# Optimization experiments

Measured on AMD Instinct MI355X. Metric: run time of the kernel, lower is better.

Reference implementation:

```python
import jax, jax.numpy as jnp
import numpy as np

D_MODEL = 2048
SSM_RANK = 8            # ultra_config.ar_ssm_max_rank = 8
FFN_RANK = D_MODEL // 64  # = 32, UltraLowRankFFN default rank
EPS = 1e-5


def setup_inputs() -> dict:
    key = jax.random.key(0)
    ks = jax.random.split(key, 10)
    d, r, rf = D_MODEL, SSM_RANK, FFN_RANK
    sc = 0.01  # xavier-ish small gain init mirroring gain=0.01
    return {
        "x": jax.random.normal(ks[0], (4, 4096, d), dtype=jnp.float32),
        # shared LayerNorm (used for both pre-norms)
        "ln_gamma": jnp.ones((d,), jnp.float32),
        "ln_beta": jnp.zeros((d,), jnp.float32),
        # AR-SSM (adaptive-rank semiseparable): input proj, per-rank decay, output proj, skip D
        "W_in": jax.random.normal(ks[1], (d, r), jnp.float32) * (1.0 / np.sqrt(d)),
        "b_in": jnp.zeros((r,), jnp.float32),
        "decay_logit": jax.random.normal(ks[2], (r,), jnp.float32),
        "W_out": jax.random.normal(ks[3], (r, d), jnp.float32) * (1.0 / np.sqrt(r)),
        "b_out": jnp.zeros((d,), jnp.float32),
        "D_skip": jax.random.normal(ks[4], (d,), jnp.float32) * 0.1,
        # Ultra low-rank FFN
        "W_down": jax.random.normal(ks[5], (d, rf), jnp.float32) * sc,
        "b_down": jnp.zeros((rf,), jnp.float32),
        "W_up": jax.random.normal(ks[6], (rf, d), jnp.float32) * sc,
        "b_up": jnp.zeros((d,), jnp.float32),
    }


def _layernorm(x, gamma, beta):
    mu = jnp.mean(x, axis=-1, keepdims=True)
    var = jnp.var(x, axis=-1, keepdims=True)
    return (x - mu) * jax.lax.rsqrt(var + EPS) * gamma + beta


def _ssm_scan(u, decay):
    # h_t = decay * h_{t-1} + u_t ; u: [B,S,r], decay: [r]
    a = jnp.broadcast_to(decay, u.shape)

    def combine(e1, e2):
        a1, b1 = e1
        a2, b2 = e2
        return a1 * a2, a2 * b1 + b2

    _, h = jax.lax.associative_scan(combine, (a, u), axis=1)
    return h  # [B,S,r]


def reference(x, ln_gamma, ln_beta, W_in, b_in, decay_logit, W_out, b_out,
              D_skip, W_down, b_down, W_up, b_up):
    # --- AR-SSM sub-block (pre-norm) ---
    xn = _layernorm(x, ln_gamma, ln_beta)
    u = jnp.einsum("bsd,dr->bsr", xn, W_in) + b_in          # low-rank input proj
    decay = jax.nn.sigmoid(decay_logit)                       # per-rank decay in (0,1)
    h = _ssm_scan(u, decay)                                   # semiseparable scan
    x_ar = jnp.einsum("bsr,rd->bsd", h, W_out) + b_out + xn * D_skip
    x = x + x_ar
    # --- Ultra low-rank FFN sub-block (same shared norm) ---
    xn2 = _layernorm(x, ln_gamma, ln_beta)
    hf = jax.nn.relu(jnp.einsum("bsd,dr->bsr", xn2, W_down) + b_down)
    x_ffn = jnp.einsum("bsr,rd->bsd", hf, W_up) + b_up
    return x + x_ffn
```

## Files before the change

### kernel.cpp

```cpp
#include <hip/hip_runtime.h>
#include <cstdint>
#include <cstddef>

#define D_MODEL 2048
#define EPSF 1e-5f

#define WS_UT    0
#define WS_MU1   131072
#define WS_RSIG1 147456
#define WS_WDT   163840
#define WS_WINF  229376
#define WS_C     245760
#define WS_D     245792
#define WS_CIN   245824
#define WS_DIN   245832

__device__ __forceinline__ float4 ld4(const float* __restrict__ p) {
    return *(const float4*)p;
}
__device__ __forceinline__ void st4(float* __restrict__ p, float4 v) {
    *(float4*)p = v;
}
__device__ __forceinline__ int bitrev6(int l) {
    return ((l & 1) << 5) | ((l & 2) << 3) | ((l & 4) << 1) |
           ((l & 8) >> 1) | ((l & 16) >> 3) | ((l & 32) >> 5);
}
__device__ __forceinline__ int bitrev4(int l) {
    return ((l & 1) << 3) | ((l & 2) << 1) | ((l & 4) >> 1) | ((l & 8) >> 3);
}

__global__ __launch_bounds__(64) void k0_prep(
    const float* __restrict__ Win, const float* __restrict__ b_in,
    const float* __restrict__ Wd, const float* __restrict__ gamma,
    const float* __restrict__ beta, const float* __restrict__ bd,
    float* __restrict__ ws)
{
    const int t = threadIdx.x;
    const int blk = blockIdx.x;
    if (blk < 8) {
        __shared__ float tile[64 * 33];
        const int gblk = blk;
        for (int cc = 0; cc < 4; ++cc) {
            const int ibase = gblk * 256 + cc * 64;
#pragma unroll
            for (int m = 0; m < 32; ++m) {
                const int e = m * 64 + t;
                const int il = e >> 5, j = e & 31;
                tile[il * 33 + j] = Wd[(size_t)ibase * 32 + e];
            }
            __syncthreads();
#pragma unroll
            for (int j = 0; j < 32; ++j) {
                const int i = ibase + t;
                ws[WS_WDT + (size_t)j * 2048 + i] = gamma[i] * tile[t * 33 + j];
            }
            __syncthreads();
        }
    } else if (blk == 8) {
        const int j = t & 31, h = t >> 5;
        float cacc = 0.f, dacc = 0.f;
        for (int k = 0; k < 1024; ++k) {
            const int i = h * 1024 + k;
            const float w = Wd[(size_t)i * 32 + j];
            cacc = fmaf(gamma[i], w, cacc);
            dacc = fmaf(beta[i], w, dacc);
        }
        cacc += __shfl_xor(cacc, 32, 64);
        dacc += __shfl_xor(dacc, 32, 64);
        if (t < 32) {
            ws[WS_C + j] = cacc;
            ws[WS_D + j] = dacc + bd[j];
        }
    } else {
        float cj[8], dj[8];
#pragma unroll
        for (int j = 0; j < 8; ++j) { cj[j] = 0.f; dj[j] = 0.f; }
        for (int k = 0; k < 32; ++k) {
            const int i = k * 64 + t;
            const float g = gamma[i], b = beta[i];
            float4 w0 = ld4(Win + (size_t)i * 8);
            float4 w1 = ld4(Win + (size_t)i * 8 + 4);
            st4(ws + WS_WINF + (size_t)i * 8,
                make_float4(g * w0.x, g * w0.y, g * w0.z, g * w0.w));
            st4(ws + WS_WINF + (size_t)i * 8 + 4,
                make_float4(g * w1.x, g * w1.y, g * w1.z, g * w1.w));
            cj[0] = fmaf(g, w0.x, cj[0]); cj[1] = fmaf(g, w0.y, cj[1]);
            cj[2] = fmaf(g, w0.z, cj[2]); cj[3] = fmaf(g, w0.w, cj[3]);
            cj[4] = fmaf(g, w1.x, cj[4]); cj[5] = fmaf(g, w1.y, cj[5]);
            cj[6] = fmaf(g, w1.z, cj[6]); cj[7] = fmaf(g, w1.w, cj[7]);
            dj[0] = fmaf(b, w0.x, dj[0]); dj[1] = fmaf(b, w0.y, dj[1]);
            dj[2] = fmaf(b, w0.z, dj[2]); dj[3] = fmaf(b, w0.w, dj[3]);
            dj[4] = fmaf(b, w1.x, dj[4]); dj[5] = fmaf(b, w1.y, dj[5]);
            dj[6] = fmaf(b, w1.z, dj[6]); dj[7] = fmaf(b, w1.w, dj[7]);
        }
#pragma unroll
        for (int off = 1; off < 64; off <<= 1) {
#pragma unroll
            for (int j = 0; j < 8; ++j) {
                cj[j] += __shfl_xor(cj[j], off, 64);
                dj[j] += __shfl_xor(dj[j], off, 64);
            }
        }
        if (t == 0) {
#pragma unroll
            for (int j = 0; j < 8; ++j) {
                ws[WS_CIN + j] = cj[j];
                ws[WS_DIN + j] = dj[j] + b_in[j];
            }
        }
    }
}

__global__ __launch_bounds__(256, 4) void k1_ln_u(
    const float* __restrict__ x, float* __restrict__ ws)
{
    __shared__ float red[8][4][12];
    const int t = threadIdx.x;
    const int wv = t >> 6, lane = t & 63;
    const int row0 = blockIdx.x * 8;
    const int i0 = t * 8;

    float winf[64];
#pragma unroll
    for (int q = 0; q < 16; ++q) {
        float4 v = ld4(ws + WS_WINF + (size_t)i0 * 8 + q * 4);
        winf[q*4+0] = v.x; winf[q*4+1] = v.y; winf[q*4+2] = v.z; winf[q*4+3] = v.w;
    }
    float4 xa = ld4(x + (size_t)row0 * D_MODEL + i0);
    float4 xb = ld4(x + (size_t)row0 * D_MODEL + i0 + 4);
#pragma unroll 1
    for (int rr = 0; rr < 8; ++rr) {
        float xc[8];
        xc[0]=xa.x; xc[1]=xa.y; xc[2]=xa.z; xc[3]=xa.w;
        xc[4]=xb.x; xc[5]=xb.y; xc[6]=xb.z; xc[7]=xb.w;
        if (rr < 7) {
            const float* xr = x + (size_t)(row0 + rr + 1) * D_MODEL + i0;
            xa = ld4(xr);
            xb = ld4(xr + 4);
        }
        float vals[16];
#pragma unroll
        for (int v = 0; v < 16; ++v) vals[v] = 0.f;
#pragma unroll
        for (int i = 0; i < 8; ++i) {
            const float xi = xc[i];
            vals[0] += xi;
            vals[1] = fmaf(xi, xi, vals[1]);
#pragma unroll
            for (int j = 0; j < 8; ++j)
                vals[2+j] = fmaf(xi, winf[i*8 + j], vals[2+j]);
        }
        int count = 16;
#pragma unroll
        for (int step = 1; step <= 32; step <<= 1) {
            if (count > 1) {
                const int half = count >> 1;
                const bool up = (lane & step) != 0;
#pragma unroll
                for (int k = 0; k < 8; ++k) {
                    if (k < half) {
                        float send = vals[up ? k : k + half];
                        float keep = vals[up ? k + half : k];
                        vals[k] = keep + __shfl_xor(send, step, 64);
                    }
                }
                count = half;
            } else {
                vals[0] += __shfl_xor(vals[0], step, 64);
            }
        }
        if (lane < 16) {
            const int v = bitrev4(lane);
            if (v < 10) red[rr][wv][v] = vals[0];
        }
    }
    __syncthreads();
    if (t < 64) {
        const int row = t >> 3, j = t & 7;
        float s_ = 0.f, q_ = 0.f, uraw = 0.f;
#pragma unroll
        for (int w = 0; w < 4; ++w) {
            s_   += red[row][w][0];
            q_   += red[row][w][1];
            uraw += red[row][w][2 + j];
        }
        const float mu = s_ * (1.f / D_MODEL);
        const float var = q_ * (1.f / D_MODEL) - mu * mu;
        const float rs = rsqrtf(var + EPSF);
        const float u = fmaf(rs, fmaf(-mu, ws[WS_CIN + j], uraw), ws[WS_DIN + j]);
        const int grow = row0 + row;
        const int bb = grow >> 12, s0 = grow & 4095;
        ws[WS_UT + ((size_t)bb * 8 + j) * 4096 + s0] = u;
        if (j == 0) {
            ws[WS_MU1 + grow] = mu;
            ws[WS_RSIG1 + grow] = rs;
        }
    }
}

__global__ __launch_bounds__(64) void k2_scan(
    const float* __restrict__ logit, float* __restrict__ ws)
{
    const int t = threadIdx.x;
    const int blk = blockIdx.x;
    const int b = blk >> 3, r = blk & 7;
    const float a = 1.f / (1.f + expf(-logit[r]));
    float* u = ws + WS_UT + ((size_t)b * 8 + r) * 4096 + t * 64;
    float v[64];
#pragma unroll
    for (int q = 0; q < 16; ++q) {
        float4 w = ld4(u + q * 4);
        v[q*4]=w.x; v[q*4+1]=w.y; v[q*4+2]=w.z; v[q*4+3]=w.w;
    }
    float c = 0.f;
#pragma unroll
    for (int k = 0; k < 64; ++k) { c = fmaf(a, c, v[k]); v[k] = c; }
    float A = a;
#pragma unroll
    for (int i = 0; i < 6; ++i) A *= A;
    float Bv = c, Aa = A;
#pragma unroll
    for (int off = 1; off < 64; off <<= 1) {
        float Ap = __shfl_up(Aa, off, 64);
        float Bp = __shfl_up(Bv, off, 64);
        if (t >= off) { Bv = fmaf(Aa, Bp, Bv); Aa *= Ap; }
    }
    float P = __shfl_up(Bv, 1, 64);
    if (t == 0) P = 0.f;
    float f = a * P;
#pragma unroll
    for (int k = 0; k < 64; ++k) { v[k] += f; f *= a; }
#pragma unroll
    for (int q = 0; q < 16; ++q)
        st4(u + q * 4, make_float4(v[q*4], v[q*4+1], v[q*4+2], v[q*4+3]));
}

__global__ __launch_bounds__(256, 2) void k3_fused(
    const float* __restrict__ x, const float* __restrict__ gamma,
    const float* __restrict__ beta, const float* __restrict__ Wout,
    const float* __restrict__ b_out, const float* __restrict__ Dsk,
    const float* __restrict__ Wu, const float* __restrict__ bu,
    float* __restrict__ out, float* __restrict__ ws)
{
    __shared__ float Y[8 * 2048];
    __shared__ float sh_h[8][8];
    __shared__ float smu1[8], srs1[8];
    __shared__ float smu2[8], srs2[8];
    __shared__ float red2[16][4];
    __shared__ float shf[8 * 32];
    const int t = threadIdx.x;
    const int blk = blockIdx.x;
    const int row0 = blk * 8;
    const int wv = t >> 6, lane = t & 63;

    if (t < 64) {
        const int r_ = t >> 3, j_ = t & 7;
        const int grow = row0 + r_;
        const int bb = grow >> 12, s = grow & 4095;
        sh_h[r_][j_] = ws[WS_UT + ((size_t)bb * 8 + j_) * 4096 + s];
        if (j_ == 0) {
            smu1[r_] = ws[WS_MU1 + grow];
            srs1[r_] = ws[WS_RSIG1 + grow];
        }
    }
    __syncthreads();

    float hreg[64];
#pragma unroll
    for (int r = 0; r < 8; ++r) {
        float4 h0 = ld4(&sh_h[r][0]);
        float4 h1 = ld4(&sh_h[r][4]);
        hreg[r*8+0]=h0.x; hreg[r*8+1]=h0.y; hreg[r*8+2]=h0.z; hreg[r*8+3]=h0.w;
        hreg[r*8+4]=h1.x; hreg[r*8+5]=h1.y; hreg[r*8+6]=h1.z; hreg[r*8+7]=h1.w;
    }

    float sum[8], ssq[8];
#pragma unroll
    for (int r = 0; r < 8; ++r) { sum[r] = 0.f; ssq[r] = 0.f; }

#pragma unroll 1
    for (int pass = 0; pass < 2; ++pass) {
        const int c = pass * 1024 + t * 4;
        const float4 g = ld4(gamma + c), bt = ld4(beta + c);
        const float4 bo = ld4(b_out + c), dk = ld4(Dsk + c);
        float4 wo[8];
#pragma unroll
        for (int j = 0; j < 8; ++j) wo[j] = ld4(Wout + (size_t)j * D_MODEL + c);
#pragma unroll
        for (int r = 0; r < 8; ++r) {
            const float4 xv = ld4(x + (size_t)(row0 + r) * D_MODEL + c);
            const float mu1 = smu1[r], rs1 = srs1[r];
            float4 acc = bo;
#pragma unroll
            for (int j = 0; j < 8; ++j) {
                const float hj = hreg[r*8 + j];
                acc.x = fmaf(hj, wo[j].x, acc.x);
                acc.y = fmaf(hj, wo[j].y, acc.y);
                acc.z = fmaf(hj, wo[j].z, acc.z);
                acc.w = fmaf(hj, wo[j].w, acc.w);
            }
            float4 xn;
            xn.x = fmaf((xv.x - mu1) * rs1, g.x, bt.x);
            xn.y = fmaf((xv.y - mu1) * rs1, g.y, bt.y);
            xn.z = fmaf((xv.z - mu1) * rs1, g.z, bt.z);
            xn.w = fmaf((xv.w - mu1) * rs1, g.w, bt.w);
            acc.x = fmaf(xn.x, dk.x, acc.x);
            acc.y = fmaf(xn.y, dk.y, acc.y);
            acc.z = fmaf(xn.z, dk.z, acc.z);
            acc.w = fmaf(xn.w, dk.w, acc.w);
            float4 x2;
            x2.x = xv.x + acc.x; x2.y = xv.y + acc.y;
            x2.z = xv.z + acc.z; x2.w = xv.w + acc.w;
            st4(&Y[r * 2048 + c], x2);
            sum[r] += x2.x + x2.y + x2.z + x2.w;
            ssq[r] = fmaf(x2.x, x2.x, ssq[r]); ssq[r] = fmaf(x2.y, x2.y, ssq[r]);
            ssq[r] = fmaf(x2.z, x2.z, ssq[r]); ssq[r] = fmaf(x2.w, x2.w, ssq[r]);
        }
    }
    {
        float vals[16];
#pragma unroll
        for (int r = 0; r < 8; ++r) { vals[r] = sum[r]; vals[8+r] = ssq[r]; }
        int count = 16;
#pragma unroll
        for (int step = 1; step <= 32; step <<= 1) {
            if (count > 1) {
                const int half = count >> 1;
                const bool up = (lane & step) != 0;
#pragma unroll
                for (int k = 0; k < 8; ++k) {
                    if (k < half) {
                        float send = vals[up ? k : k + half];
                        float keep = vals[up ? k + half : k];
                        vals[k] = keep + __shfl_xor(send, step, 64);
                    }
                }
                count = half;
            } else {
                vals[0] += __shfl_xor(vals[0], step, 64);
            }
        }
        if (lane < 16) red2[bitrev4(lane)][wv] = vals[0];
    }
    __syncthreads();
    if (t < 8) {
        float s_ = red2[t][0] + red2[t][1] + red2[t][2] + red2[t][3];
        float q_ = red2[8+t][0] + red2[8+t][1] + red2[8+t][2] + red2[8+t][3];
        const float mu2 = s_ * (1.f / D_MODEL);
        const float var = q_ * (1.f / D_MODEL) - mu2 * mu2;
        smu2[t] = mu2;
        srs2[t] = rsqrtf(var + EPSF);
    }
    __syncthreads();

    const int jb = wv * 8;
    float p[64];
#pragma unroll
    for (int v = 0; v < 64; ++v) p[v] = 0.f;
    float4 wb[8], wbn[8];
#pragma unroll
    for (int jj = 0; jj < 8; ++jj)
        wb[jj] = ld4(ws + WS_WDT + (size_t)(jb + jj) * 2048 + lane * 4);
#pragma unroll 1
    for (int q = 0; q < 8; ++q) {
        const int ip = q * 256 + lane * 4;
        if (q < 7) {
#pragma unroll
            for (int jj = 0; jj < 8; ++jj)
                wbn[jj] = ld4(ws + WS_WDT + (size_t)(jb + jj) * 2048 + ip + 256);
        }
        float4 yv[8];
#pragma unroll
        for (int rr = 0; rr < 8; ++rr) yv[rr] = ld4(&Y[rr * 2048 + ip]);
#pragma unroll
        for (int jj = 0; jj < 8; ++jj) {
#pragma unroll
            for (int rr = 0; rr < 8; ++rr) {
                p[rr*8+jj] = fmaf(yv[rr].x, wb[jj].x, p[rr*8+jj]);
                p[rr*8+jj] = fmaf(yv[rr].y, wb[jj].y, p[rr*8+jj]);
                p[rr*8+jj] = fmaf(yv[rr].z, wb[jj].z, p[rr*8+jj]);
                p[rr*8+jj] = fmaf(yv[rr].w, wb[jj].w, p[rr*8+jj]);
            }
        }
#pragma unroll
        for (int jj = 0; jj < 8; ++jj) wb[jj] = wbn[jj];
    }
    {
        int count = 64;
#pragma unroll
        for (int step = 1; step <= 32; step <<= 1) {
            const int half = count >> 1;
            const bool up = (lane & step) != 0;
#pragma unroll
            for (int k = 0; k < 32; ++k) {
                if (k < half) {
                    float send = p[up ? k : k + half];
                    float keep = p[up ? k + half : k];
                    p[k] = keep + __shfl_xor(send, step, 64);
                }
            }
            count = half;
        }
    }
    {
        const int v = bitrev6(lane);
        const int r_ = v >> 3, j_ = v & 7;
        const float mu2r = smu2[r_], rs2r = srs2[r_];
        const float cj = ws[WS_C + jb + j_], dj = ws[WS_D + jb + j_];
        shf[r_ * 32 + jb + j_] =
            fmaxf(0.f, fmaf(rs2r, fmaf(-mu2r, cj, p[0]), dj));
    }
    __syncthreads();

    const int c0 = t * 4;
    float4 a0[8], a1[8];
    const float4 bu0 = ld4(bu + c0), bu1 = ld4(bu + 1024 + c0);
#pragma unroll
    for (int rr = 0; rr < 8; ++rr) {
        float4 y0 = ld4(&Y[rr * 2048 + c0]);
        float4 y1 = ld4(&Y[rr * 2048 + 1024 + c0]);
        a0[rr] = make_float4(y0.x + bu0.x, y0.y + bu0.y, y0.z + bu0.z, y0.w + bu0.w);
        a1[rr] = make_float4(y1.x + bu1.x, y1.y + bu1.y, y1.z + bu1.z, y1.w + bu1.w);
    }
    float4 w0[4], w1[4], w0n[4], w1n[4];
#pragma unroll
    for (int jj = 0; jj < 4; ++jj) {
        w0[jj] = ld4(Wu + (size_t)jj * D_MODEL + c0);
        w1[jj] = ld4(Wu + (size_t)jj * D_MODEL + 1024 + c0);
    }
#pragma unroll 1
    for (int jc = 0; jc < 8; ++jc) {
        if (jc < 7) {
#pragma unroll
            for (int jj = 0; jj < 4; ++jj) {
                w0n[jj] = ld4(Wu + (size_t)((jc+1)*4 + jj) * D_MODEL + c0);
                w1n[jj] = ld4(Wu + (size_t)((jc+1)*4 + jj) * D_MODEL + 1024 + c0);
            }
        }
        float4 hq[8];
#pragma unroll
        for (int rr = 0; rr < 8; ++rr) hq[rr] = ld4(&shf[rr * 32 + jc * 4]);
#pragma unroll
        for (int jj = 0; jj < 4; ++jj) {
#pragma unroll
            for (int rr = 0; rr < 8; ++rr) {
                const float hval = (jj == 0) ? hq[rr].x : (jj == 1) ? hq[rr].y
                                 : (jj == 2) ? hq[rr].z : hq[rr].w;
                a0[rr].x = fmaf(hval, w0[jj].x, a0[rr].x);
                a0[rr].y = fmaf(hval, w0[jj].y, a0[rr].y);
                a0[rr].z = fmaf(hval, w0[jj].z, a0[rr].z);
                a0[rr].w = fmaf(hval, w0[jj].w, a0[rr].w);
                a1[rr].x = fmaf(hval, w1[jj].x, a1[rr].x);
                a1[rr].y = fmaf(hval, w1[jj].y, a1[rr].y);
                a1[rr].z = fmaf(hval, w1[jj].z, a1[rr].z);
                a1[rr].w = fmaf(hval, w1[jj].w, a1[rr].w);
            }
        }
#pragma unroll
        for (int jj = 0; jj < 4; ++jj) { w0[jj] = w0n[jj]; w1[jj] = w1n[jj]; }
    }
#pragma unroll
    for (int rr = 0; rr < 8; ++rr) {
        float* orow = out + (size_t)(row0 + rr) * D_MODEL;
        st4(orow + c0, a0[rr]);
        st4(orow + 1024 + c0, a1[rr]);
    }
}

extern "C" void kernel_launch(void* const* d_in, const int* in_sizes, int n_in,
                              void* d_out, int out_size, void* d_ws, size_t ws_size,
                              hipStream_t stream) {
    const float* x      = (const float*)d_in[0];
    const float* gamma  = (const float*)d_in[1];
    const float* beta   = (const float*)d_in[2];
    const float* Win    = (const float*)d_in[3];
    const float* b_in   = (const float*)d_in[4];
    const float* logit  = (const float*)d_in[5];
    const float* Wout   = (const float*)d_in[6];
    const float* b_out  = (const float*)d_in[7];
    const float* Dsk    = (const float*)d_in[8];
    const float* Wd     = (const float*)d_in[9];
    const float* bd     = (const float*)d_in[10];
    const float* Wu     = (const float*)d_in[11];
    const float* bu     = (const float*)d_in[12];
    float* out = (float*)d_out;
    float* ws  = (float*)d_ws;

    hipLaunchKernelGGL(k0_prep, dim3(10),   dim3(64),  0, stream,
                       Win, b_in, Wd, gamma, beta, bd, ws);
    hipLaunchKernelGGL(k1_ln_u, dim3(2048), dim3(256), 0, stream, x, ws);
    hipLaunchKernelGGL(k2_scan, dim3(32),   dim3(64),  0, stream, logit, ws);
    hipLaunchKernelGGL(k3_fused, dim3(2048), dim3(256), 0, stream,
                       x, gamma, beta, Wout, b_out, Dsk, Wu, bu, out, ws);
}
```

Measured before the change: 502.0 us.

## Distribute FFN down-proj constant reductions and process 16 rows per LN block

The serial single-block reduction of gamma·W_down and beta·W_down in the prep kernel is replaced by per-block partial sums computed from the already-staged shared-memory tile. These partials are combined by an extra block in the scan kernel. The first LayerNorm/input-projection kernel now handles 16 rows per block with coalesced strided columns (half as many blocks), amortizing the weight register loads. The epilogue is reorganized so 16 threads each write all 8 rank outputs. This aims to cut the long serial prep tail and the per-block overhead of the LN kernel, at the cost of fewer blocks for latency hiding.

```diff
diff --git a/kernel.cpp b/kernel.cpp
--- a/kernel.cpp
+++ b/kernel.cpp
@@ -14,6 +14,7 @@
 #define WS_D     245792
 #define WS_CIN   245824
 #define WS_DIN   245832
+#define WS_CP    245840
 
 __device__ __forceinline__ float4 ld4(const float* __restrict__ p) {
     return *(const float4*)p;
@@ -39,38 +40,38 @@
     const int blk = blockIdx.x;
     if (blk < 8) {
         __shared__ float tile[64 * 33];
-        const int gblk = blk;
+        __shared__ float sg[64], sb[64];
+        float part = 0.f;
         for (int cc = 0; cc < 4; ++cc) {
-            const int ibase = gblk * 256 + cc * 64;
+            const int ibase = blk * 256 + cc * 64;
 #pragma unroll
             for (int m = 0; m < 32; ++m) {
                 const int e = m * 64 + t;
                 const int il = e >> 5, j = e & 31;
                 tile[il * 33 + j] = Wd[(size_t)ibase * 32 + e];
             }
+            sg[t] = gamma[ibase + t];
+            sb[t] = beta[ibase + t];
             __syncthreads();
 #pragma unroll
-            for (int j = 0; j < 32; ++j) {
-                const int i = ibase + t;
-                ws[WS_WDT + (size_t)j * 2048 + i] = gamma[i] * tile[t * 33 + j];
+            for (int j = 0; j < 32; ++j)
+                ws[WS_WDT + (size_t)j * 2048 + ibase + t] = sg[t] * tile[t * 33 + j];
+            {
+                const int j = t & 31;
+                const float* wvec = (t < 32) ? sg : sb;
+                float a0 = 0.f, a1 = 0.f, a2 = 0.f, a3 = 0.f;
+#pragma unroll
+                for (int il = 0; il < 64; il += 4) {
+                    a0 = fmaf(wvec[il+0], tile[(il+0) * 33 + j], a0);
+                    a1 = fmaf(wvec[il+1], tile[(il+1) * 33 + j], a1);
+                    a2 = fmaf(wvec[il+2], tile[(il+2) * 33 + j], a2);
+                    a3 = fmaf(wvec[il+3], tile[(il+3) * 33 + j], a3);
+                }
+                part += (a0 + a1) + (a2 + a3);
             }
             __syncthreads();
         }
-    } else if (blk == 8) {
-        const int j = t & 31, h = t >> 5;
-        float cacc = 0.f, dacc = 0.f;
-        for (int k = 0; k < 1024; ++k) {
-            const int i = h * 1024 + k;
-            const float w = Wd[(size_t)i * 32 + j];
-            cacc = fmaf(gamma[i], w, cacc);
-            dacc = fmaf(beta[i], w, dacc);
-        }
-        cacc += __shfl_xor(cacc, 32, 64);
-        dacc += __shfl_xor(dacc, 32, 64);
-        if (t < 32) {
-            ws[WS_C + j] = cacc;
-            ws[WS_D + j] = dacc + bd[j];
-        }
+        ws[WS_CP + blk * 64 + t] = part;
     } else {
         float cj[8], dj[8];
 #pragma unroll
@@ -114,41 +115,49 @@
 __global__ __launch_bounds__(256, 4) void k1_ln_u(
     const float* __restrict__ x, float* __restrict__ ws)
 {
-    __shared__ float red[8][4][12];
+    __shared__ float red[16][4][12];
     const int t = threadIdx.x;
     const int wv = t >> 6, lane = t & 63;
-    const int row0 = blockIdx.x * 8;
-    const int i0 = t * 8;
+    const int row0 = blockIdx.x * 16;
+    const int c0 = wv * 512 + lane * 4;
 
     float winf[64];
 #pragma unroll
-    for (int q = 0; q < 16; ++q) {
-        float4 v = ld4(ws + WS_WINF + (size_t)i0 * 8 + q * 4);
-        winf[q*4+0] = v.x; winf[q*4+1] = v.y; winf[q*4+2] = v.z; winf[q*4+3] = v.w;
-    }
-    float4 xa = ld4(x + (size_t)row0 * D_MODEL + i0);
-    float4 xb = ld4(x + (size_t)row0 * D_MODEL + i0 + 4);
+    for (int rep = 0; rep < 2; ++rep) {
+        const int ib = c0 + rep * 256;
+#pragma unroll
+        for (int q = 0; q < 8; ++q) {
+            float4 v = ld4(ws + WS_WINF + (size_t)ib * 8 + q * 4);
+            winf[rep*32 + q*4 + 0] = v.x; winf[rep*32 + q*4 + 1] = v.y;
+            winf[rep*32 + q*4 + 2] = v.z; winf[rep*32 + q*4 + 3] = v.w;
+        }
+    }
+    float4 xa = ld4(x + (size_t)row0 * D_MODEL + c0);
+    float4 xb = ld4(x + (size_t)row0 * D_MODEL + c0 + 256);
 #pragma unroll 1
-    for (int rr = 0; rr < 8; ++rr) {
+    for (int rr = 0; rr < 16; ++rr) {
         float xc[8];
         xc[0]=xa.x; xc[1]=xa.y; xc[2]=xa.z; xc[3]=xa.w;
         xc[4]=xb.x; xc[5]=xb.y; xc[6]=xb.z; xc[7]=xb.w;
-        if (rr < 7) {
-            const float* xr = x + (size_t)(row0 + rr + 1) * D_MODEL + i0;
+        if (rr < 15) {
+            const float* xr = x + (size_t)(row0 + rr + 1) * D_MODEL + c0;
             xa = ld4(xr);
-            xb = ld4(xr + 4);
+            xb = ld4(xr + 256);
         }
         float vals[16];
 #pragma unroll
         for (int v = 0; v < 16; ++v) vals[v] = 0.f;
 #pragma unroll
-        for (int i = 0; i < 8; ++i) {
-            const float xi = xc[i];
-            vals[0] += xi;
-            vals[1] = fmaf(xi, xi, vals[1]);
-#pragma unroll
-            for (int j = 0; j < 8; ++j)
-                vals[2+j] = fmaf(xi, winf[i*8 + j], vals[2+j]);
+        for (int rep = 0; rep < 2; ++rep) {
+#pragma unroll
+            for (int di = 0; di < 4; ++di) {
+                const float xi = xc[rep*4 + di];
+                vals[0] += xi;
+                vals[1] = fmaf(xi, xi, vals[1]);
+#pragma unroll
+                for (int j = 0; j < 8; ++j)
+                    vals[2+j] = fmaf(xi, winf[rep*32 + di*8 + j], vals[2+j]);
+            }
         }
         int count = 16;
 #pragma unroll
@@ -175,34 +184,48 @@
         }
     }
     __syncthreads();
-    if (t < 64) {
-        const int row = t >> 3, j = t & 7;
-        float s_ = 0.f, q_ = 0.f, uraw = 0.f;
+    if (t < 16) {
+        const int grow = row0 + t;
+        float s_ = 0.f, q_ = 0.f, uraw[8];
+#pragma unroll
+        for (int j = 0; j < 8; ++j) uraw[j] = 0.f;
 #pragma unroll
         for (int w = 0; w < 4; ++w) {
-            s_   += red[row][w][0];
-            q_   += red[row][w][1];
-            uraw += red[row][w][2 + j];
+            s_ += red[t][w][0];
+            q_ += red[t][w][1];
+#pragma unroll
+            for (int j = 0; j < 8; ++j) uraw[j] += red[t][w][2 + j];
         }
         const float mu = s_ * (1.f / D_MODEL);
         const float var = q_ * (1.f / D_MODEL) - mu * mu;
         const float rs = rsqrtf(var + EPSF);
-        const float u = fmaf(rs, fmaf(-mu, ws[WS_CIN + j], uraw), ws[WS_DIN + j]);
-        const int grow = row0 + row;
         const int bb = grow >> 12, s0 = grow & 4095;
-        ws[WS_UT + ((size_t)bb * 8 + j) * 4096 + s0] = u;
-        if (j == 0) {
-            ws[WS_MU1 + grow] = mu;
-            ws[WS_RSIG1 + grow] = rs;
-        }
+#pragma unroll
+        for (int j = 0; j < 8; ++j) {
+            const float u = fmaf(rs, fmaf(-mu, ws[WS_CIN + j], uraw[j]),
+                                 ws[WS_DIN + j]);
+            ws[WS_UT + ((size_t)bb * 8 + j) * 4096 + s0] = u;
+        }
+        ws[WS_MU1 + grow] = mu;
+        ws[WS_RSIG1 + grow] = rs;
     }
 }
 
 __global__ __launch_bounds__(64) void k2_scan(
-    const float* __restrict__ logit, float* __restrict__ ws)
+    const float* __restrict__ logit, const float* __restrict__ bd,
+    float* __restrict__ ws)
 {
     const int t = threadIdx.x;
     const int blk = blockIdx.x;
+    if (blk == 32) {
+        const int j = t & 31;
+        float s = 0.f;
+#pragma unroll
+        for (int g = 0; g < 8; ++g) s += ws[WS_CP + g * 64 + (t < 32 ? j : 32 + j)];
+        if (t < 32) ws[WS_C + j] = s;
+        else        ws[WS_D + j] = s + bd[j];
+        return;
+    }
     const int b = blk >> 3, r = blk & 7;
     const float a = 1.f / (1.f + expf(-logit[r]));
     float* u = ws + WS_UT + ((size_t)b * 8 + r) * 4096 + t * 64;
@@ -486,10 +509,10 @@
     float* out = (float*)d_out;
     float* ws  = (float*)d_ws;
 
-    hipLaunchKernelGGL(k0_prep, dim3(10),   dim3(64),  0, stream,
+    hipLaunchKernelGGL(k0_prep, dim3(9),    dim3(64),  0, stream,
                        Win, b_in, Wd, gamma, beta, bd, ws);
-    hipLaunchKernelGGL(k1_ln_u, dim3(2048), dim3(256), 0, stream, x, ws);
-    hipLaunchKernelGGL(k2_scan, dim3(32),   dim3(64),  0, stream, logit, ws);
+    hipLaunchKernelGGL(k1_ln_u, dim3(1024), dim3(256), 0, stream, x, ws);
+    hipLaunchKernelGGL(k2_scan, dim3(33),   dim3(64),  0, stream, logit, bd, ws);
     hipLaunchKernelGGL(k3_fused, dim3(2048), dim3(256), 0, stream,
                        x, gamma, beta, Wout, b_out, Dsk, Wu, bu, out, ws);
 }
```

New measurement: 464.7 us. 1.08x faster.
